# Performance work log

Measured on AMD Instinct MI355X. Metric: run time of the kernel, lower is better.

Reference implementation:

```python
import jax, jax.numpy as jnp
import numpy as np

VOCAB = 30000      # min(30000, 50000) from __init__
NUM_HASHES = 768   # output_dim
B, S = 64, 1024


def _next_prime(n: int) -> int:
    def is_prime(k):
        if k <= 1:
            return False
        for i in range(2, int(k ** 0.5) + 1):
            if k % i == 0:
                return False
        return True
    while not is_prime(n):
        n += 1
    return n


def setup_inputs() -> dict:
    key = jax.random.key(0)
    k1, _ = jax.random.split(key)
    input_ids = jax.random.randint(k1, (B, S), 0, VOCAB, dtype=jnp.int32)
    attention_mask = jnp.ones((B, S), dtype=jnp.int32)

    # Hash function params (buffers in the torch module), deterministic via numpy.
    prime = _next_prime(VOCAB)
    rng = np.random.default_rng(0)
    a = rng.integers(1, prime - 1, size=(NUM_HASHES, 1), dtype=np.int64)
    b = rng.integers(0, prime - 1, size=(NUM_HASHES, 1), dtype=np.int64)
    vocab_idx = np.arange(VOCAB, dtype=np.int64)[None, :]
    hashed_vocab = ((a * vocab_idx + b) % prime).astype(np.float32)  # (H, V)
    return {
        "input_ids": input_ids,
        "attention_mask": attention_mask,
        "hashed_vocab": jnp.asarray(hashed_vocab),
    }


def reference(input_ids, attention_mask, hashed_vocab):
    vocab_size = hashed_vocab.shape[1]
    # Token is used iff attended AND 100 < id < vocab_size (same filter as torch).
    valid = (attention_mask == 1) & (input_ids > 100) & (input_ids < vocab_size)  # (B,S)
    ids_safe = jnp.where(valid, input_ids, 0)
    # Gather per-token hashes: (B, S, H). min over a multiset ignores duplicates,
    # so this equals the torch bow-vector + masked-min over the full vocab.
    gathered = hashed_vocab.T[ids_safe]
    masked = jnp.where(valid[..., None], gathered, jnp.inf)
    signatures = jnp.min(masked, axis=1)  # (B, H)
    # F.normalize(p=2, dim=-1) with eps=1e-12
    norm = jnp.linalg.norm(signatures, axis=-1, keepdims=True)
    return signatures / jnp.maximum(norm, 1e-12)
```

## Files before the change

kernel.cpp:

```cpp
#include <hip/hip_runtime.h>
#include <stdint.h>


#define BATCH  64
#define SEQ    1024
#define NH     768
#define VOCABI 30000
#define PRIME  30011u
#define MAGIC  586191265u

__device__ __forceinline__ unsigned int hmod(unsigned int aa, unsigned int bb,
                                             unsigned int id) {
  const unsigned int x = __umul24(aa, id) + bb;
  const unsigned int q = __umulhi(x, MAGIC) >> 12;
  return x - __umul24(q, PRIME);
}

__global__ void __launch_bounds__(512) minhash_fused(
    const int* __restrict__ ids, const int* __restrict__ mask,
    const float* __restrict__ hv, float* __restrict__ sig) {
  __shared__ unsigned int s_ids[SEQ];
  __shared__ unsigned int s_red[512];
  __shared__ unsigned int s_cnt;
  const int tid = threadIdx.x;
  const int b = blockIdx.y;

  if (tid == 0) s_cnt = 0;
  __syncthreads();
#pragma unroll
  for (int i = 0; i < SEQ / 512; ++i) {
    const int s = tid + i * 512;
    const int id = ids[b * SEQ + s];
    const int m  = mask[b * SEQ + s];
    if (m == 1 && id > 100 && id < VOCABI)
      s_ids[atomicAdd(&s_cnt, 1u)] = (unsigned int)id;
  }
  __syncthreads();
  const unsigned int c = s_cnt;
  const unsigned int pad = (c > 0) ? s_ids[0] : 0u;
  for (unsigned int s = c + tid; s < SEQ; s += 512) s_ids[s] = pad;

  const int lane = tid & 63;
  const int chunk = tid >> 6;
  const int h = blockIdx.x * 64 + lane;
  const float h0 = hv[(size_t)h * VOCABI];
  const float h1 = hv[(size_t)h * VOCABI + 1];
  const unsigned int bb = (unsigned int)h0;
  int ai = (int)h1 - (int)h0;
  if (ai < 0) ai += (int)PRIME;
  const unsigned int aa = (unsigned int)ai;
  __syncthreads();

  const uint4* __restrict__ p4 = (const uint4*)(s_ids + chunk * (SEQ / 8));
  unsigned int acc = 0xFFFFFFFFu;
#pragma unroll 8
  for (int j = 0; j < SEQ / 8 / 4; ++j) {
    const uint4 v = p4[j];
    acc = min(acc, hmod(aa, bb, v.x));
    acc = min(acc, hmod(aa, bb, v.y));
    acc = min(acc, hmod(aa, bb, v.z));
    acc = min(acc, hmod(aa, bb, v.w));
  }

  s_red[chunk * 64 + lane] = acc;
  __syncthreads();
  if (tid < 64) {
    unsigned int m = s_red[tid];
#pragma unroll
    for (int k = 1; k < 8; ++k) m = min(m, s_red[k * 64 + tid]);
    sig[b * NH + blockIdx.x * 64 + tid] = (c > 0) ? (float)m : INFINITY;
  }
}

__global__ void __launch_bounds__(256) norm_kernel(
    const float* __restrict__ sig, float* __restrict__ out) {
  const int b = blockIdx.x;
  const int t = threadIdx.x;
  const float v0 = sig[b * NH + t];
  const float v1 = sig[b * NH + 256 + t];
  const float v2 = sig[b * NH + 512 + t];
  float ss = v0 * v0 + v1 * v1 + v2 * v2;
#pragma unroll
  for (int off = 32; off > 0; off >>= 1) ss += __shfl_down(ss, off, 64);
  __shared__ float red[4];
  if ((t & 63) == 0) red[t >> 6] = ss;
  __syncthreads();
  const float total = red[0] + red[1] + red[2] + red[3];
  const float inv = 1.0f / fmaxf(sqrtf(total), 1e-12f);
  out[b * NH + t] = v0 * inv;
  out[b * NH + 256 + t] = v1 * inv;
  out[b * NH + 512 + t] = v2 * inv;
}

extern "C" void kernel_launch(void* const* d_in, const int* in_sizes, int n_in,
                              void* d_out, int out_size, void* d_ws, size_t ws_size,
                              hipStream_t stream) {
  const int* input_ids = (const int*)d_in[0];
  const int* attn_mask = (const int*)d_in[1];
  const float* hv      = (const float*)d_in[2];
  float* out           = (float*)d_out;
  float* sig           = (float*)d_ws;

  minhash_fused<<<dim3(NH / 64, BATCH), 512, 0, stream>>>(input_ids, attn_mask, hv, sig);
  norm_kernel<<<BATCH, 256, 0, stream>>>(sig, out);
}
```

Before: 126.8 us.

## Fuse normalization into minhash kernel via last-block counter; ballot-based compaction

Replaces the separate norm kernel with a last-block-done pattern: each block bumps a per-batch atomic counter, and the final block for that batch row reads all signatures and writes the L2-normalized output. Token compaction now uses a wave ballot and prefix popcount, so there is one shared atomic per wave instead of one per valid token. The aim is to remove the second kernel launch and cut shared-memory atomic contention. In exchange it adds a memset launch, thread fences and a serialized tail in one block per batch row.

```diff
diff --git a/kernel.cpp b/kernel.cpp
--- a/kernel.cpp
+++ b/kernel.cpp
@@ -8,6 +8,7 @@
 #define VOCABI 30000
 #define PRIME  30011u
 #define MAGIC  586191265u
+#define NBLK_PER_B (NH / 64)
 
 __device__ __forceinline__ unsigned int hmod(unsigned int aa, unsigned int bb,
                                              unsigned int id) {
@@ -16,33 +17,46 @@
   return x - __umul24(q, PRIME);
 }
 
-__global__ void __launch_bounds__(512) minhash_fused(
+__global__ void __launch_bounds__(512) minhash_one(
     const int* __restrict__ ids, const int* __restrict__ mask,
-    const float* __restrict__ hv, float* __restrict__ sig) {
+    const float* __restrict__ hv, float* __restrict__ sig,
+    unsigned int* __restrict__ cnts, float* __restrict__ out) {
+  const int tid  = threadIdx.x;
+  const int lane = tid & 63;
+  const int wv   = tid >> 6;
+  const int hc   = blockIdx.x;
+  const int b    = blockIdx.y;
+
   __shared__ unsigned int s_ids[SEQ];
   __shared__ unsigned int s_red[512];
   __shared__ unsigned int s_cnt;
-  const int tid = threadIdx.x;
-  const int b = blockIdx.y;
+  __shared__ int s_last;
+  __shared__ float s_ss[8];
 
   if (tid == 0) s_cnt = 0;
   __syncthreads();
+
 #pragma unroll
   for (int i = 0; i < SEQ / 512; ++i) {
-    const int s = tid + i * 512;
+    const int s  = tid + i * 512;
     const int id = ids[b * SEQ + s];
     const int m  = mask[b * SEQ + s];
-    if (m == 1 && id > 100 && id < VOCABI)
-      s_ids[atomicAdd(&s_cnt, 1u)] = (unsigned int)id;
+    const bool valid = (m == 1) && (id > 100) && (id < VOCABI);
+    const unsigned long long bal = __ballot(valid);
+    unsigned int base = 0;
+    if (lane == 0) base = atomicAdd(&s_cnt, (unsigned int)__popcll(bal));
+    base = (unsigned int)__shfl((int)base, 0, 64);
+    if (valid) {
+      const int nb = __popcll(bal & ((1ull << lane) - 1ull));
+      s_ids[base + nb] = (unsigned int)id;
+    }
   }
   __syncthreads();
   const unsigned int c = s_cnt;
   const unsigned int pad = (c > 0) ? s_ids[0] : 0u;
   for (unsigned int s = c + tid; s < SEQ; s += 512) s_ids[s] = pad;
 
-  const int lane = tid & 63;
-  const int chunk = tid >> 6;
-  const int h = blockIdx.x * 64 + lane;
+  const int h = hc * 64 + lane;
   const float h0 = hv[(size_t)h * VOCABI];
   const float h1 = hv[(size_t)h * VOCABI + 1];
   const unsigned int bb = (unsigned int)h0;
@@ -51,7 +65,7 @@
   const unsigned int aa = (unsigned int)ai;
   __syncthreads();
 
-  const uint4* __restrict__ p4 = (const uint4*)(s_ids + chunk * (SEQ / 8));
+  const uint4* __restrict__ p4 = (const uint4*)(s_ids + wv * (SEQ / 8));
   unsigned int acc = 0xFFFFFFFFu;
 #pragma unroll 8
   for (int j = 0; j < SEQ / 8 / 4; ++j) {
@@ -61,35 +75,39 @@
     acc = min(acc, hmod(aa, bb, v.z));
     acc = min(acc, hmod(aa, bb, v.w));
   }
-
-  s_red[chunk * 64 + lane] = acc;
+  s_red[wv * 64 + lane] = acc;
   __syncthreads();
   if (tid < 64) {
     unsigned int m = s_red[tid];
 #pragma unroll
     for (int k = 1; k < 8; ++k) m = min(m, s_red[k * 64 + tid]);
-    sig[b * NH + blockIdx.x * 64 + tid] = (c > 0) ? (float)m : INFINITY;
+    sig[b * NH + hc * 64 + tid] = (c > 0) ? (float)m : INFINITY;
   }
-}
 
-__global__ void __launch_bounds__(256) norm_kernel(
-    const float* __restrict__ sig, float* __restrict__ out) {
-  const int b = blockIdx.x;
-  const int t = threadIdx.x;
-  const float v0 = sig[b * NH + t];
-  const float v1 = sig[b * NH + 256 + t];
-  const float v2 = sig[b * NH + 512 + t];
-  float ss = v0 * v0 + v1 * v1 + v2 * v2;
+  __threadfence();
+  __syncthreads();
+  if (tid == 0) {
+    const unsigned int old = atomicAdd(&cnts[b], 1u);
+    s_last = (old == NBLK_PER_B - 1);
+  }
+  __syncthreads();
+  if (!s_last) return;
+  __threadfence();
+
+  const volatile float* vs = sig + b * NH;
+  const float v0 = vs[tid];
+  const float v1 = (tid < NH - 512) ? vs[512 + tid] : 0.0f;
+  float ss = v0 * v0 + v1 * v1;
 #pragma unroll
   for (int off = 32; off > 0; off >>= 1) ss += __shfl_down(ss, off, 64);
-  __shared__ float red[4];
-  if ((t & 63) == 0) red[t >> 6] = ss;
+  if (lane == 0) s_ss[wv] = ss;
   __syncthreads();
-  const float total = red[0] + red[1] + red[2] + red[3];
+  float total = 0.f;
+#pragma unroll
+  for (int k = 0; k < 8; ++k) total += s_ss[k];
   const float inv = 1.0f / fmaxf(sqrtf(total), 1e-12f);
-  out[b * NH + t] = v0 * inv;
-  out[b * NH + 256 + t] = v1 * inv;
-  out[b * NH + 512 + t] = v2 * inv;
+  out[b * NH + tid] = v0 * inv;
+  if (tid < NH - 512) out[b * NH + 512 + tid] = v1 * inv;
 }
 
 extern "C" void kernel_launch(void* const* d_in, const int* in_sizes, int n_in,
@@ -99,8 +117,11 @@
   const int* attn_mask = (const int*)d_in[1];
   const float* hv      = (const float*)d_in[2];
   float* out           = (float*)d_out;
-  float* sig           = (float*)d_ws;
 
-  minhash_fused<<<dim3(NH / 64, BATCH), 512, 0, stream>>>(input_ids, attn_mask, hv, sig);
-  norm_kernel<<<BATCH, 256, 0, stream>>>(sig, out);
+  unsigned int* cnts = (unsigned int*)d_ws;
+  float* sig         = (float*)((uint8_t*)d_ws + 256);
+
+  hipMemsetAsync(cnts, 0, BATCH * sizeof(unsigned int), stream);
+  minhash_one<<<dim3(NBLK_PER_B, BATCH), 512, 0, stream>>>(
+      input_ids, attn_mask, hv, sig, cnts, out);
 }
```

Measured after the change: 237.5 us. +87.4%, slower.
